# Kernel optimization log

Hardware: AMD Instinct MI355X
Metric: run time of the kernel (lower is better)

## Reference

```python
import jax, jax.numpy as jnp
import numpy as np

N_CLASSES = 1000
FEAT_DIM = 1024
PROJ_DIM = 256
BATCH = 32
NUM_SUPPORT = 8192


def setup_inputs() -> dict:
    key = jax.random.key(0)
    k1, k2, k3, k4 = jax.random.split(key, 4)
    x = jax.random.normal(k1, (BATCH, FEAT_DIM), dtype=jnp.float32)
    sx = jax.random.normal(k2, (NUM_SUPPORT, FEAT_DIM), dtype=jnp.float32)
    # xavier_uniform_ on (1, feat_dim, proj_dim): bound = sqrt(6/(feat+proj))
    bound = float(np.sqrt(6.0 / (FEAT_DIM + PROJ_DIM)))
    proj_weight = jax.random.uniform(k3, (FEAT_DIM, PROJ_DIM), dtype=jnp.float32,
                                     minval=-bound, maxval=bound)
    sy = jax.random.randint(k4, (NUM_SUPPORT,), 0, N_CLASSES, dtype=jnp.int64)
    return {"x": x, "sx": sx, "proj_weight": proj_weight, "sy": sy}


def reference(x, sx, proj_weight, sy):
    # One-hot support labels: (N, C)
    sy_oh = jax.nn.one_hot(sy, N_CLASSES, dtype=jnp.float32)
    # Low-rank projection (shared support set -> project once; identical math
    # to the original's per-batch bmm with a repeated weight).
    xq = x @ proj_weight            # (b, p)
    sxp = sx @ proj_weight          # (N, p)
    # Euclidean kernel: scores = -||xq_i - sxp_j||^2, shape (b, N)
    x_sq = jnp.sum(xq * xq, axis=-1, keepdims=True)       # (b, 1)
    s_sq = jnp.sum(sxp * sxp, axis=-1)[None, :]           # (1, N)
    scores = -(x_sq + s_sq - 2.0 * (xq @ sxp.T))          # (b, N)
    probs = jax.nn.softmax(scores, axis=-1)               # (b, N)
    out = probs @ sy_oh                                   # (b, C)
    return jnp.log(out + 1e-12)
```

## Files before the change

kernel.cpp:

```cpp
#include <hip/hip_runtime.h>
#include <hip/hip_bf16.h>
#include <math.h>

#define N_CLASSES 1000
#define FEAT_DIM 1024
#define PROJ_DIM 256
#define BATCH 32
#define NUM_SUPPORT 8192

#define PA_BLOCKS 8192
#define PW_BLOCKS 16
#define PX_BLOCKS 256

typedef __attribute__((ext_vector_type(8))) _Float16 f16x8;
typedef __attribute__((ext_vector_type(4))) _Float16 f16x4;
typedef __attribute__((ext_vector_type(2))) _Float16 f16x2;
typedef __attribute__((ext_vector_type(4))) float f32x4;

__device__ inline unsigned enc_f(float f) {
  unsigned u = __float_as_uint(f);
  return (u & 0x80000000u) ? ~u : (u | 0x80000000u);
}
__device__ inline float dec_f(unsigned e) {
  return (e & 0x80000000u) ? __uint_as_float(e & 0x7FFFFFFFu)
                           : __uint_as_float(~e);
}

__global__ __launch_bounds__(256) void prelude_kernel(
    const float* __restrict__ sx, const float* __restrict__ W,
    const float* __restrict__ x, _Float16* __restrict__ A1,
    _Float16* __restrict__ W1, float* __restrict__ xq,
    unsigned* __restrict__ rowmaxU) {
  __shared__ float part[256];
  __shared__ _Float16 Lw[256][66];
  const int bid = blockIdx.x;
  const int t = threadIdx.x;

  if (bid < PA_BLOCKS) {
    const int r = bid;
    const float4 v = *(const float4*)&sx[(size_t)r * FEAT_DIM + t * 4];
    f16x4 h = {(_Float16)v.x, (_Float16)v.y, (_Float16)v.z, (_Float16)v.w};
    *(f16x4*)&A1[(size_t)r * FEAT_DIM + t * 4] = h;
  } else if (bid < PA_BLOCKS + PW_BLOCKS) {
    const int k0 = (bid - PA_BLOCKS) * 64;
#pragma unroll 8
    for (int kk = 0; kk < 64; kk++) {
      Lw[t][kk] = (_Float16)W[(size_t)(k0 + kk) * PROJ_DIM + t];
    }
    __syncthreads();
#pragma unroll
    for (int i = 0; i < 8; i++) {
      *(f16x8*)&W1[(size_t)t * FEAT_DIM + k0 + i * 8] =
          *(f16x8*)&Lw[t][i * 8];
    }
  } else {
    const int pxb = bid - PA_BLOCKS - PW_BLOCKS;
    const int b = pxb >> 3, cc = pxb & 7;
    if (pxb == 0 && t < BATCH) rowmaxU[t] = 0u;

    const int col = t & 31, ks = t >> 5;
    const int gc = cc * 32 + col;
    const int k0 = ks * 128;
    float s = 0.f;
#pragma unroll 8
    for (int k = 0; k < 128; k++) {
      s = fmaf(x[(size_t)b * FEAT_DIM + k0 + k],
               W[(size_t)(k0 + k) * PROJ_DIM + gc], s);
    }
    part[t] = s;
    __syncthreads();
    if (t < 32) {
      float acc = 0.f;
#pragma unroll
      for (int i = 0; i < 8; i++) acc += part[i * 32 + t];
      xq[(size_t)b * PROJ_DIM + cc * 32 + t] = acc;
    }
  }
}

__global__ __launch_bounds__(256) void sxp_mfma_kernel(
    const _Float16* __restrict__ A1, const _Float16* __restrict__ W1,
    _Float16* __restrict__ sxp16) {
  __shared__ _Float16 At[128 * 64];
  __shared__ _Float16 Bt[64 * 64];

  const int tid = threadIdx.x;
  const int w = tid >> 6;
  const int lane = tid & 63;
  const int bm = (blockIdx.x & 63) * 128;
  const int bn = (blockIdx.x >> 6) * 64;
  const int wm = w & 1, wn = w >> 1;
  const int m16 = lane & 15, quad = lane >> 4;
  const int lrow8 = lane >> 3;
  const int g = (lane & 7) ^ lrow8;

  f32x4 acc[4][2];
#pragma unroll
  for (int mt = 0; mt < 4; mt++)
#pragma unroll
    for (int nt = 0; nt < 2; nt++) acc[mt][nt] = (f32x4){0.f, 0.f, 0.f, 0.f};

  for (int kb = 0; kb < FEAT_DIM; kb += 64) {
#pragma unroll
    for (int i = 0; i < 4; i++) {
      const int row = w * 32 + i * 8 + lrow8;
      const _Float16* gp = A1 + (size_t)(bm + row) * FEAT_DIM + kb + g * 8;
      __builtin_amdgcn_global_load_lds(
          (const __attribute__((address_space(1))) void*)gp,
          (__attribute__((address_space(3))) void*)(At + (w * 32 + i * 8) * 64),
          16, 0, 0);
    }
#pragma unroll
    for (int i = 0; i < 2; i++) {
      const int nrow = w * 16 + i * 8 + lrow8;
      const _Float16* gp = W1 + (size_t)(bn + nrow) * FEAT_DIM + kb + g * 8;
      __builtin_amdgcn_global_load_lds(
          (const __attribute__((address_space(1))) void*)gp,
          (__attribute__((address_space(3))) void*)(Bt + (w * 16 + i * 8) * 64),
          16, 0, 0);
    }
    __syncthreads();

#pragma unroll
    for (int s = 0; s < 2; s++) {
      const int slot = (s * 4 + quad) ^ (m16 & 7);
      f16x8 af[4], bf[2];
#pragma unroll
      for (int mt = 0; mt < 4; mt++) {
        const int row = wm * 64 + mt * 16 + m16;
        af[mt] = *(f16x8*)&At[row * 64 + slot * 8];
      }
#pragma unroll
      for (int nt = 0; nt < 2; nt++) {
        const int nrow = wn * 32 + nt * 16 + m16;
        bf[nt] = *(f16x8*)&Bt[nrow * 64 + slot * 8];
      }
#pragma unroll
      for (int mt = 0; mt < 4; mt++)
#pragma unroll
        for (int nt = 0; nt < 2; nt++)
          acc[mt][nt] = __builtin_amdgcn_mfma_f32_16x16x32_f16(
              af[mt], bf[nt], acc[mt][nt], 0, 0, 0);
    }
    __syncthreads();
  }

#pragma unroll
  for (int mt = 0; mt < 4; mt++)
#pragma unroll
    for (int nt = 0; nt < 2; nt++)
#pragma unroll
      for (int r = 0; r < 4; r++) {
        const int mg = bm + wm * 64 + mt * 16 + quad * 4 + r;
        const int ng = bn + wn * 32 + nt * 16 + m16;
        sxp16[(size_t)mg * PROJ_DIM + ng] = (_Float16)acc[mt][nt][r];
      }
}

__global__ __launch_bounds__(256) void score_kernel(
    const float* __restrict__ xq, const _Float16* __restrict__ sxp16,
    float* __restrict__ sc, unsigned* __restrict__ rowmaxU) {
  __shared__ _Float16 xqh[4 * PROJ_DIM];
  __shared__ float xsqL[4];
  __shared__ float redm[4][4];

  const int t = threadIdx.x;
  const int jc = blockIdx.x;
  const int bg = blockIdx.y;
  const int lane = t & 63, wave = t >> 6;

  float xv[4];
#pragma unroll
  for (int i = 0; i < 4; i++) {
    xv[i] = xq[(size_t)(bg * 4 + i) * PROJ_DIM + t];
    xqh[i * PROJ_DIM + t] = (_Float16)xv[i];
  }
#pragma unroll
  for (int i = 0; i < 4; i++) {
    float v = xv[i] * xv[i];
#pragma unroll
    for (int o = 1; o < 64; o <<= 1) v += __shfl_xor(v, o, 64);
    if (lane == 0) redm[i][wave] = v;
  }
  __syncthreads();
  if (t < 4) xsqL[t] = redm[t][0] + redm[t][1] + redm[t][2] + redm[t][3];
  __syncthreads();

  const int j = jc * 256 + t;
  const f16x8* __restrict__ rowp =
      (const f16x8*)(sxp16 + (size_t)j * PROJ_DIM);
  float dot[4] = {0.f, 0.f, 0.f, 0.f};
  float rsq = 0.f;

#pragma unroll 4
  for (int q = 0; q < PROJ_DIM / 8; q++) {
    const f16x8 hv = rowp[q];
    const f16x2* hp = (const f16x2*)&hv;
#pragma unroll
    for (int b = 0; b < 4; b++) {
      const f16x8 xb = *(const f16x8*)&xqh[b * PROJ_DIM + q * 8];
      const f16x2* xp = (const f16x2*)&xb;
#pragma unroll
      for (int i = 0; i < 4; i++)
        dot[b] = __builtin_amdgcn_fdot2(hp[i], xp[i], dot[b], false);
    }
#pragma unroll
    for (int i = 0; i < 4; i++)
      rsq = __builtin_amdgcn_fdot2(hp[i], hp[i], rsq, false);
  }

#pragma unroll
  for (int c = 0; c < 4; c++) {
    const float s = 2.0f * dot[c] - rsq - xsqL[c];
    sc[(size_t)(bg * 4 + c) * NUM_SUPPORT + j] = s;
    float v = s;
#pragma unroll
    for (int o = 1; o < 64; o <<= 1) v = fmaxf(v, __shfl_xor(v, o, 64));
    if (lane == 0) redm[c][wave] = v;
  }
  __syncthreads();
  if (t < 4) {
    const float m =
        fmaxf(fmaxf(redm[t][0], redm[t][1]), fmaxf(redm[t][2], redm[t][3]));
    atomicMax(&rowmaxU[bg * 4 + t], enc_f(m));
  }
}

__global__ __launch_bounds__(1024) void finish_kernel(
    const float* __restrict__ sc, const unsigned* __restrict__ rowmaxU,
    const int* __restrict__ sy, float* __restrict__ out) {
  __shared__ float cls[N_CLASSES];
  __shared__ float red[16];

  const int b = blockIdx.x;
  const int t = threadIdx.x;
  const int lane = t & 63, wave = t >> 6;
  const float m = dec_f(rowmaxU[b]);

  for (int c = t; c < N_CLASSES; c += 1024) cls[c] = 0.0f;
  __syncthreads();

  float lsum = 0.0f;
#pragma unroll
  for (int jj = 0; jj < NUM_SUPPORT / 1024; jj++) {
    const int j = jj * 1024 + t;
    const float e = expf(sc[(size_t)b * NUM_SUPPORT + j] - m);
    lsum += e;
    atomicAdd(&cls[sy[j]], e);
  }
#pragma unroll
  for (int o = 1; o < 64; o <<= 1) lsum += __shfl_xor(lsum, o, 64);
  if (lane == 0) red[wave] = lsum;
  __syncthreads();
  if (t == 0) {
    float s = 0.f;
#pragma unroll
    for (int i = 0; i < 16; i++) s += red[i];
    red[0] = s;
  }
  __syncthreads();
  const float inv = 1.0f / red[0];
  for (int c = t; c < N_CLASSES; c += 1024) {
    out[(size_t)b * N_CLASSES + c] = logf(cls[c] * inv + 1e-12f);
  }
}

extern "C" void kernel_launch(void* const* d_in, const int* in_sizes, int n_in,
                              void* d_out, int out_size, void* d_ws,
                              size_t ws_size, hipStream_t stream) {
  const float* x = (const float*)d_in[0];
  const float* sx = (const float*)d_in[1];
  const float* W = (const float*)d_in[2];
  const int* sy = (const int*)d_in[3];
  float* out = (float*)d_out;

  char* p = (char*)d_ws;
  float* xq = (float*)p;            p += (size_t)BATCH * PROJ_DIM * 4;
  unsigned* rowmaxU = (unsigned*)p; p += 128;
  _Float16* sxp16 = (_Float16*)p;   p += (size_t)NUM_SUPPORT * PROJ_DIM * 2;
  float* sc = (float*)p;            p += (size_t)BATCH * NUM_SUPPORT * 4;
  _Float16* A1 = (_Float16*)p;      p += (size_t)NUM_SUPPORT * FEAT_DIM * 2;
  _Float16* W1 = (_Float16*)p;

  prelude_kernel<<<dim3(PA_BLOCKS + PW_BLOCKS + PX_BLOCKS), dim3(256), 0,
                   stream>>>(sx, W, x, A1, W1, xq, rowmaxU);
  sxp_mfma_kernel<<<dim3(256), dim3(256), 0, stream>>>(A1, W1, sxp16);
  score_kernel<<<dim3(NUM_SUPPORT / 256, BATCH / 4), dim3(256), 0, stream>>>(
      xq, sxp16, sc, rowmaxU);
  finish_kernel<<<dim3(BATCH), dim3(1024), 0, stream>>>(sc, rowmaxU, sy, out);
}
```

Measured before the change: 130.9 us.

## Fuse support projection GEMM with score computation via atomic partial sums

Merges the sxp GEMM and the score kernel into one kernel. Each 64x64 output tile of the projection stays in LDS and is immediately dotted against a 64-wide slice of 2*xq, and the partial scores are added into a zeroed score buffer with global atomics. This removes the sxp16 round trip and one launch. The per-row x_sq term is dropped because it is constant within a softmax row, and the row max moves into the finish kernel. In exchange the code adds 4-way atomic contention per score element, a zeroing pass in the prelude, and smaller 64-row GEMM tiles remapped across XCDs to keep occupancy at 512 blocks.

Result: faster. 120.3 us (-8.1%).

```diff
diff --git a/kernel.cpp b/kernel.cpp
--- a/kernel.cpp
+++ b/kernel.cpp
@@ -1,5 +1,4 @@
 #include <hip/hip_runtime.h>
-#include <hip/hip_bf16.h>
 #include <math.h>
 
 #define N_CLASSES 1000
@@ -11,26 +10,18 @@
 #define PA_BLOCKS 8192
 #define PW_BLOCKS 16
 #define PX_BLOCKS 256
+#define PZ_BLOCKS 256
 
 typedef __attribute__((ext_vector_type(8))) _Float16 f16x8;
 typedef __attribute__((ext_vector_type(4))) _Float16 f16x4;
 typedef __attribute__((ext_vector_type(2))) _Float16 f16x2;
 typedef __attribute__((ext_vector_type(4))) float f32x4;
 
-__device__ inline unsigned enc_f(float f) {
-  unsigned u = __float_as_uint(f);
-  return (u & 0x80000000u) ? ~u : (u | 0x80000000u);
-}
-__device__ inline float dec_f(unsigned e) {
-  return (e & 0x80000000u) ? __uint_as_float(e & 0x7FFFFFFFu)
-                           : __uint_as_float(~e);
-}
-
 __global__ __launch_bounds__(256) void prelude_kernel(
     const float* __restrict__ sx, const float* __restrict__ W,
     const float* __restrict__ x, _Float16* __restrict__ A1,
-    _Float16* __restrict__ W1, float* __restrict__ xq,
-    unsigned* __restrict__ rowmaxU) {
+    _Float16* __restrict__ W1, _Float16* __restrict__ xqh2,
+    float* __restrict__ sc) {
   __shared__ float part[256];
   __shared__ _Float16 Lw[256][66];
   const int bid = blockIdx.x;
@@ -50,14 +41,11 @@
     __syncthreads();
 #pragma unroll
     for (int i = 0; i < 8; i++) {
-      *(f16x8*)&W1[(size_t)t * FEAT_DIM + k0 + i * 8] =
-          *(f16x8*)&Lw[t][i * 8];
-    }
-  } else {
+      *(f16x8*)&W1[(size_t)t * FEAT_DIM + k0 + i * 8] = *(f16x8*)&Lw[t][i * 8];
+    }
+  } else if (bid < PA_BLOCKS + PW_BLOCKS + PX_BLOCKS) {
     const int pxb = bid - PA_BLOCKS - PW_BLOCKS;
     const int b = pxb >> 3, cc = pxb & 7;
-    if (pxb == 0 && t < BATCH) rowmaxU[t] = 0u;
-
     const int col = t & 31, ks = t >> 5;
     const int gc = cc * 32 + col;
     const int k0 = ks * 128;
@@ -73,41 +61,55 @@
       float acc = 0.f;
 #pragma unroll
       for (int i = 0; i < 8; i++) acc += part[i * 32 + t];
-      xq[(size_t)b * PROJ_DIM + cc * 32 + t] = acc;
-    }
-  }
-}
-
-__global__ __launch_bounds__(256) void sxp_mfma_kernel(
+      xqh2[(size_t)b * PROJ_DIM + cc * 32 + t] = (_Float16)(2.0f * acc);
+    }
+  } else {
+    const int zb = bid - PA_BLOCKS - PW_BLOCKS - PX_BLOCKS;
+    float4 z = {0.f, 0.f, 0.f, 0.f};
+    *(float4*)&sc[(size_t)zb * 1024 + t * 4] = z;
+  }
+}
+
+__global__ __launch_bounds__(256) void gemm_score_kernel(
     const _Float16* __restrict__ A1, const _Float16* __restrict__ W1,
-    _Float16* __restrict__ sxp16) {
-  __shared__ _Float16 At[128 * 64];
+    const _Float16* __restrict__ xqh2, float* __restrict__ sc) {
+  __shared__ _Float16 At[64 * 64];
   __shared__ _Float16 Bt[64 * 64];
+  __shared__ _Float16 Sx[64 * 72];
+  __shared__ _Float16 Xl[32 * 64];
 
   const int tid = threadIdx.x;
   const int w = tid >> 6;
   const int lane = tid & 63;
-  const int bm = (blockIdx.x & 63) * 128;
-  const int bn = (blockIdx.x >> 6) * 64;
+  const int xcd = blockIdx.x & 7;
+  const int idx = blockIdx.x >> 3;
+  const int bm = (xcd * 16 + (idx & 15)) * 64;
+  const int bn = (idx >> 4) * 64;
   const int wm = w & 1, wn = w >> 1;
   const int m16 = lane & 15, quad = lane >> 4;
   const int lrow8 = lane >> 3;
   const int g = (lane & 7) ^ lrow8;
 
-  f32x4 acc[4][2];
-#pragma unroll
-  for (int mt = 0; mt < 4; mt++)
+  {
+    const int r = tid >> 3, c = tid & 7;
+    *(f16x8*)&Xl[r * 64 + c * 8] =
+        *(const f16x8*)&xqh2[(size_t)r * PROJ_DIM + bn + c * 8];
+  }
+
+  f32x4 acc[2][2];
+#pragma unroll
+  for (int mt = 0; mt < 2; mt++)
 #pragma unroll
     for (int nt = 0; nt < 2; nt++) acc[mt][nt] = (f32x4){0.f, 0.f, 0.f, 0.f};
 
   for (int kb = 0; kb < FEAT_DIM; kb += 64) {
 #pragma unroll
-    for (int i = 0; i < 4; i++) {
-      const int row = w * 32 + i * 8 + lrow8;
+    for (int i = 0; i < 2; i++) {
+      const int row = w * 16 + i * 8 + lrow8;
       const _Float16* gp = A1 + (size_t)(bm + row) * FEAT_DIM + kb + g * 8;
       __builtin_amdgcn_global_load_lds(
           (const __attribute__((address_space(1))) void*)gp,
-          (__attribute__((address_space(3))) void*)(At + (w * 32 + i * 8) * 64),
+          (__attribute__((address_space(3))) void*)(At + (w * 16 + i * 8) * 64),
           16, 0, 0);
     }
 #pragma unroll
@@ -124,10 +126,10 @@
 #pragma unroll
     for (int s = 0; s < 2; s++) {
       const int slot = (s * 4 + quad) ^ (m16 & 7);
-      f16x8 af[4], bf[2];
-#pragma unroll
-      for (int mt = 0; mt < 4; mt++) {
-        const int row = wm * 64 + mt * 16 + m16;
+      f16x8 af[2], bf[2];
+#pragma unroll
+      for (int mt = 0; mt < 2; mt++) {
+        const int row = wm * 32 + mt * 16 + m16;
         af[mt] = *(f16x8*)&At[row * 64 + slot * 8];
       }
 #pragma unroll
@@ -136,7 +138,7 @@
         bf[nt] = *(f16x8*)&Bt[nrow * 64 + slot * 8];
       }
 #pragma unroll
-      for (int mt = 0; mt < 4; mt++)
+      for (int mt = 0; mt < 2; mt++)
 #pragma unroll
         for (int nt = 0; nt < 2; nt++)
           acc[mt][nt] = __builtin_amdgcn_mfma_f32_16x16x32_f16(
@@ -146,122 +148,88 @@
   }
 
 #pragma unroll
-  for (int mt = 0; mt < 4; mt++)
+  for (int mt = 0; mt < 2; mt++)
 #pragma unroll
     for (int nt = 0; nt < 2; nt++)
 #pragma unroll
       for (int r = 0; r < 4; r++) {
-        const int mg = bm + wm * 64 + mt * 16 + quad * 4 + r;
-        const int ng = bn + wn * 32 + nt * 16 + m16;
-        sxp16[(size_t)mg * PROJ_DIM + ng] = (_Float16)acc[mt][nt][r];
+        const int jl = wm * 32 + mt * 16 + quad * 4 + r;
+        const int nl = wn * 32 + nt * 16 + m16;
+        Sx[jl * 72 + nl] = (_Float16)acc[mt][nt][r];
       }
-}
-
-__global__ __launch_bounds__(256) void score_kernel(
-    const float* __restrict__ xq, const _Float16* __restrict__ sxp16,
-    float* __restrict__ sc, unsigned* __restrict__ rowmaxU) {
-  __shared__ _Float16 xqh[4 * PROJ_DIM];
-  __shared__ float xsqL[4];
-  __shared__ float redm[4][4];
-
-  const int t = threadIdx.x;
-  const int jc = blockIdx.x;
-  const int bg = blockIdx.y;
-  const int lane = t & 63, wave = t >> 6;
-
-  float xv[4];
-#pragma unroll
-  for (int i = 0; i < 4; i++) {
-    xv[i] = xq[(size_t)(bg * 4 + i) * PROJ_DIM + t];
-    xqh[i * PROJ_DIM + t] = (_Float16)xv[i];
-  }
-#pragma unroll
-  for (int i = 0; i < 4; i++) {
-    float v = xv[i] * xv[i];
-#pragma unroll
-    for (int o = 1; o < 64; o <<= 1) v += __shfl_xor(v, o, 64);
-    if (lane == 0) redm[i][wave] = v;
-  }
   __syncthreads();
-  if (t < 4) xsqL[t] = redm[t][0] + redm[t][1] + redm[t][2] + redm[t][3];
-  __syncthreads();
-
-  const int j = jc * 256 + t;
-  const f16x8* __restrict__ rowp =
-      (const f16x8*)(sxp16 + (size_t)j * PROJ_DIM);
-  float dot[4] = {0.f, 0.f, 0.f, 0.f};
+
+  const int j = tid & 63;
+  const int bg = tid >> 6;
+  float dotb[8] = {0.f, 0.f, 0.f, 0.f, 0.f, 0.f, 0.f, 0.f};
   float rsq = 0.f;
-
-#pragma unroll 4
-  for (int q = 0; q < PROJ_DIM / 8; q++) {
-    const f16x8 hv = rowp[q];
+#pragma unroll
+  for (int c = 0; c < 8; c++) {
+    const f16x8 hv = *(const f16x8*)&Sx[j * 72 + c * 8];
     const f16x2* hp = (const f16x2*)&hv;
-#pragma unroll
-    for (int b = 0; b < 4; b++) {
-      const f16x8 xb = *(const f16x8*)&xqh[b * PROJ_DIM + q * 8];
-      const f16x2* xp = (const f16x2*)&xb;
-#pragma unroll
-      for (int i = 0; i < 4; i++)
-        dot[b] = __builtin_amdgcn_fdot2(hp[i], xp[i], dot[b], false);
-    }
 #pragma unroll
     for (int i = 0; i < 4; i++)
       rsq = __builtin_amdgcn_fdot2(hp[i], hp[i], rsq, false);
-  }
-
-#pragma unroll
-  for (int c = 0; c < 4; c++) {
-    const float s = 2.0f * dot[c] - rsq - xsqL[c];
-    sc[(size_t)(bg * 4 + c) * NUM_SUPPORT + j] = s;
-    float v = s;
-#pragma unroll
-    for (int o = 1; o < 64; o <<= 1) v = fmaxf(v, __shfl_xor(v, o, 64));
-    if (lane == 0) redm[c][wave] = v;
-  }
-  __syncthreads();
-  if (t < 4) {
-    const float m =
-        fmaxf(fmaxf(redm[t][0], redm[t][1]), fmaxf(redm[t][2], redm[t][3]));
-    atomicMax(&rowmaxU[bg * 4 + t], enc_f(m));
+#pragma unroll
+    for (int b8 = 0; b8 < 8; b8++) {
+      const f16x8 xv = *(const f16x8*)&Xl[(bg * 8 + b8) * 64 + c * 8];
+      const f16x2* xp = (const f16x2*)&xv;
+#pragma unroll
+      for (int i = 0; i < 4; i++)
+        dotb[b8] = __builtin_amdgcn_fdot2(hp[i], xp[i], dotb[b8], false);
+    }
+  }
+#pragma unroll
+  for (int b8 = 0; b8 < 8; b8++) {
+    atomicAdd(&sc[(size_t)(bg * 8 + b8) * NUM_SUPPORT + bm + j],
+              dotb[b8] - rsq);
   }
 }
 
 __global__ __launch_bounds__(1024) void finish_kernel(
-    const float* __restrict__ sc, const unsigned* __restrict__ rowmaxU,
-    const int* __restrict__ sy, float* __restrict__ out) {
+    const float* __restrict__ sc, const int* __restrict__ sy,
+    float* __restrict__ out) {
   __shared__ float cls[N_CLASSES];
-  __shared__ float red[16];
+  __shared__ float redm[16];
+  __shared__ float reds[16];
 
   const int b = blockIdx.x;
   const int t = threadIdx.x;
   const int lane = t & 63, wave = t >> 6;
-  const float m = dec_f(rowmaxU[b]);
-
-  for (int c = t; c < N_CLASSES; c += 1024) cls[c] = 0.0f;
+
+  float v[8];
+  float m = -1e30f;
+#pragma unroll
+  for (int jj = 0; jj < 8; jj++) {
+    v[jj] = sc[(size_t)b * NUM_SUPPORT + jj * 1024 + t];
+    m = fmaxf(m, v[jj]);
+  }
+#pragma unroll
+  for (int o = 1; o < 64; o <<= 1) m = fmaxf(m, __shfl_xor(m, o, 64));
+  if (lane == 0) redm[wave] = m;
+  if (t < N_CLASSES) cls[t] = 0.0f;
   __syncthreads();
+  float gm = redm[0];
+#pragma unroll
+  for (int i = 1; i < 16; i++) gm = fmaxf(gm, redm[i]);
 
   float lsum = 0.0f;
 #pragma unroll
-  for (int jj = 0; jj < NUM_SUPPORT / 1024; jj++) {
-    const int j = jj * 1024 + t;
-    const float e = expf(sc[(size_t)b * NUM_SUPPORT + j] - m);
+  for (int jj = 0; jj < 8; jj++) {
+    const float e = expf(v[jj] - gm);
     lsum += e;
-    atomicAdd(&cls[sy[j]], e);
+    atomicAdd(&cls[sy[jj * 1024 + t]], e);
   }
 #pragma unroll
   for (int o = 1; o < 64; o <<= 1) lsum += __shfl_xor(lsum, o, 64);
-  if (lane == 0) red[wave] = lsum;
+  if (lane == 0) reds[wave] = lsum;
   __syncthreads();
-  if (t == 0) {
-    float s = 0.f;
-#pragma unroll
-    for (int i = 0; i < 16; i++) s += red[i];
-    red[0] = s;
-  }
-  __syncthreads();
-  const float inv = 1.0f / red[0];
-  for (int c = t; c < N_CLASSES; c += 1024) {
-    out[(size_t)b * N_CLASSES + c] = logf(cls[c] * inv + 1e-12f);
+  float total = 0.f;
+#pragma unroll
+  for (int i = 0; i < 16; i++) total += reds[i];
+  const float inv = 1.0f / total;
+  if (t < N_CLASSES) {
+    out[(size_t)b * N_CLASSES + t] = logf(cls[t] * inv + 1e-12f);
   }
 }
 
@@ -275,17 +243,13 @@
   float* out = (float*)d_out;
 
   char* p = (char*)d_ws;
-  float* xq = (float*)p;            p += (size_t)BATCH * PROJ_DIM * 4;
-  unsigned* rowmaxU = (unsigned*)p; p += 128;
-  _Float16* sxp16 = (_Float16*)p;   p += (size_t)NUM_SUPPORT * PROJ_DIM * 2;
-  float* sc = (float*)p;            p += (size_t)BATCH * NUM_SUPPORT * 4;
-  _Float16* A1 = (_Float16*)p;      p += (size_t)NUM_SUPPORT * FEAT_DIM * 2;
-  _Float16* W1 = (_Float16*)p;
-
-  prelude_kernel<<<dim3(PA_BLOCKS + PW_BLOCKS + PX_BLOCKS), dim3(256), 0,
-                   stream>>>(sx, W, x, A1, W1, xq, rowmaxU);
-  sxp_mfma_kernel<<<dim3(256), dim3(256), 0, stream>>>(A1, W1, sxp16);
-  score_kernel<<<dim3(NUM_SUPPORT / 256, BATCH / 4), dim3(256), 0, stream>>>(
-      xq, sxp16, sc, rowmaxU);
-  finish_kernel<<<dim3(BATCH), dim3(1024), 0, stream>>>(sc, rowmaxU, sy, out);
-}
+  float* sc = (float*)p;          p += (size_t)BATCH * NUM_SUPPORT * 4;
+  _Float16* A1 = (_Float16*)p;    p += (size_t)NUM_SUPPORT * FEAT_DIM * 2;
+  _Float16* W1 = (_Float16*)p;    p += (size_t)PROJ_DIM * FEAT_DIM * 2;
+  _Float16* xqh2 = (_Float16*)p;
+
+  prelude_kernel<<<dim3(PA_BLOCKS + PW_BLOCKS + PX_BLOCKS + PZ_BLOCKS),
+                   dim3(256), 0, stream>>>(sx, W, x, A1, W1, xqh2, sc);
+  gemm_score_kernel<<<dim3(512), dim3(256), 0, stream>>>(A1, W1, xqh2, sc);
+  finish_kernel<<<dim3(BATCH), dim3(1024), 0, stream>>>(sc, sy, out);
+}
```
